# Optimization experiments

Hardware: AMD Instinct MI355X
Metric: run time of the kernel (lower is better)

The kernel has to match this reference:

```python
import jax, jax.numpy as jnp
import numpy as np

KH, KW = 3, 3
STRIDE = (1, 1)
PADDING = (1, 1)
DILATION = (1, 1)


def setup_inputs() -> dict:
    key = jax.random.key(0)
    k1, k2, k3, k4, k5 = jax.random.split(key, 5)
    B, Cin, H, W = 8, 64, 128, 128
    Cout = 64
    Ho, Wo = 128, 128  # stride 1, pad 1, k=3 -> same spatial size
    K = KH * KW
    return {
        "input": jax.random.normal(k1, (B, Cin, H, W), dtype=jnp.float32),
        "offset": jax.random.normal(k2, (B, 2 * K, Ho, Wo), dtype=jnp.float32),
        "mask": jax.random.uniform(k3, (B, K, Ho, Wo), dtype=jnp.float32),
        "weight": jax.random.normal(k4, (Cout, Cin, KH, KW), dtype=jnp.float32) * 0.05,
        "bias": jax.random.normal(k5, (Cout,), dtype=jnp.float32) * 0.05,
    }


def _deform_conv2d(x, weight, offset, mask, bias, stride, padding, dilation):
    B, Cin, H, W = x.shape
    Cout, Cing, kh, kw = weight.shape
    G = Cin // Cing                      # weight groups
    K = kh * kw
    Goff = offset.shape[1] // (2 * K)    # offset groups
    Ho, Wo = offset.shape[2], offset.shape[3]
    Cg = Cin // Goff                     # channels per offset group
    sh, sw = stride
    ph, pw = padding
    dh, dw = dilation

    # offsets laid out as (y, x) pairs per kernel tap per offset group
    off = offset.reshape(B, Goff, K, 2, Ho, Wo)
    ky = (jnp.arange(K) // kw).astype(jnp.float32) * dh   # [K]
    kx = (jnp.arange(K) % kw).astype(jnp.float32) * dw
    gy = (jnp.arange(Ho).astype(jnp.float32) * sh - ph)    # [Ho]
    gx = (jnp.arange(Wo).astype(jnp.float32) * sw - pw)
    # sampling positions: [B, Goff, K, Ho, Wo]
    py = off[:, :, :, 0] + ky[None, None, :, None, None] + gy[None, None, None, :, None]
    px = off[:, :, :, 1] + kx[None, None, :, None, None] + gx[None, None, None, None, :]

    y0 = jnp.floor(py)
    x0 = jnp.floor(px)
    ly = py - y0
    lx = px - x0
    y0i = y0.astype(jnp.int32)
    x0i = x0.astype(jnp.int32)

    x_g = x.reshape(B, Goff, Cg, H * W)

    def gather(yi, xi):
        # zero padding outside the image
        valid = (yi >= 0) & (yi < H) & (xi >= 0) & (xi < W)
        yc = jnp.clip(yi, 0, H - 1)
        xc = jnp.clip(xi, 0, W - 1)
        idx = (yc * W + xc).reshape(B, Goff, K * Ho * Wo)
        v = jnp.take_along_axis(x_g, idx[:, :, None, :], axis=3)  # [B,Goff,Cg,K*Ho*Wo]
        return v * valid.reshape(B, Goff, 1, K * Ho * Wo)

    w00 = ((1 - ly) * (1 - lx)).reshape(B, Goff, 1, K * Ho * Wo)
    w01 = ((1 - ly) * lx).reshape(B, Goff, 1, K * Ho * Wo)
    w10 = (ly * (1 - lx)).reshape(B, Goff, 1, K * Ho * Wo)
    w11 = (ly * lx).reshape(B, Goff, 1, K * Ho * Wo)

    sampled = w00 * gather(y0i, x0i)
    sampled = sampled + w01 * gather(y0i, x0i + 1)
    sampled = sampled + w10 * gather(y0i + 1, x0i)
    sampled = sampled + w11 * gather(y0i + 1, x0i + 1)
    sampled = sampled.reshape(B, Goff, Cg, K, Ho, Wo)

    if mask is not None:
        sampled = sampled * mask.reshape(B, Goff, 1, K, Ho, Wo)

    # grouped conv accumulate
    sampled = sampled.reshape(B, G, Cing, K, Ho, Wo)
    w = weight.reshape(G, Cout // G, Cing, K)
    out = jnp.einsum('gock,bgcksq->bgosq', w, sampled).reshape(B, Cout, Ho, Wo)
    if bias is not None:
        out = out + bias[None, :, None, None]
    return out


def reference(input, offset, mask, weight, bias):
    return _deform_conv2d(input, weight, offset, mask, bias, STRIDE, PADDING, DILATION)
```

## Files before the change

### kernel.cpp

```cpp
#include <hip/hip_runtime.h>
#include <hip/hip_fp16.h>

#define HH 128
#define WW 128
#define HW (HH*WW)
#define XT_BYTES ((size_t)8 * HW * 64 * 2)
#define WT_BYTES ((size_t)9 * 2 * 4 * 64 * 8 * 2)

typedef __attribute__((ext_vector_type(8))) short short8;
typedef __attribute__((ext_vector_type(4))) float f32x4;
typedef _Float16 half8 __attribute__((ext_vector_type(8)));

static __device__ __forceinline__ unsigned short f2bf(float f) {
    unsigned int u = __float_as_uint(f);
    u += 0x7fffu + ((u >> 16) & 1u);
    return (unsigned short)(u >> 16);
}
static __device__ __forceinline__ unsigned pkrtz(float lo, float hi) {
    auto r = __builtin_amdgcn_cvt_pkrtz(lo, hi);
    return *(unsigned*)&r;
}

__global__ void wtrans_kernel(const float* __restrict__ w, unsigned short* __restrict__ wt) {
    int i = blockIdx.x * 256 + threadIdx.x;
    if (i < 9 * 2 * 4 * 64 * 8) {
        int e  = i & 7;
        int l  = (i >> 3) & 63;
        int wv = (i >> 9) & 3;
        int kf = (i >> 11) & 1;
        int k  = i >> 12;
        int co = wv * 16 + (l & 15);
        int c  = kf * 32 + (l >> 4) * 8 + e;
        __half hh = __float2half_rn(w[(co * 64 + c) * 9 + k]);
        wt[i] = __half_as_ushort(hh);
    }
}

__global__ __launch_bounds__(256) void xtrans_kernel(const float* __restrict__ x,
                                                     unsigned int* __restrict__ xt32) {
    __shared__ float tile[64][65];
    const int bid = blockIdx.x;
    const int b   = bid >> 8;
    const int hw0 = (bid & 255) << 6;
    const int t   = threadIdx.x;
    #pragma unroll
    for (int i = 0; i < 16; ++i) {
        int idx = (i << 8) + t;
        int c = idx >> 6, j = idx & 63;
        tile[c][j] = x[(size_t)(((b << 6) + c) << 14) + hw0 + j];
    }
    __syncthreads();
    #pragma unroll
    for (int i = 0; i < 8; ++i) {
        int idx = (i << 8) + t;
        int cp = idx & 31, hw = idx >> 5;
        xt32[((size_t)((b << 14) + hw0 + hw) << 5) + cp] =
            pkrtz(tile[2 * cp][hw], tile[2 * cp + 1][hw]);
    }
}

__global__ __launch_bounds__(256, 6) void deform_nhwc(
    const unsigned short* __restrict__ xt,
    const float* __restrict__ off,
    const float* __restrict__ msk,
    const unsigned short* __restrict__ wt,
    const float* __restrict__ bias,
    float* __restrict__ out)
{
    __shared__ __align__(16) unsigned char smem[25600];
    ushort4* moSu = (ushort4*)(smem + 16384);
    uint2*   mwH  = (uint2*)(smem + 20992);

    const int t   = threadIdx.x;
    const int bid = blockIdx.x;
    const int b   = bid & 7;
    const int rem = bid >> 3;
    const int ho  = rem >> 1;
    const int wo0 = (rem & 1) << 6;
    const int l   = t & 63;
    const int wv  = __builtin_amdgcn_readfirstlane(t >> 6);

    for (int i = t; i < 9 * 64; i += 256) {
        int p = i & 63;
        int k = i >> 6;
        int wo = wo0 + p;
        int obase = ((b * 18 + 2 * k) * HH + ho) * WW + wo;
        float oy = off[obase];
        float ox = off[obase + HW];
        float m  = msk[((b * 9 + k) * HH + ho) * WW + wo];
        float py = oy + (float)(k / 3) + (float)(ho - 1);
        float px = ox + (float)(k % 3) + (float)(wo - 1);
        float fy = floorf(py), fx = floorf(px);
        float ly = py - fy,    lx = px - fx;
        int y0 = (int)fy, x0 = (int)fx;
        int y1 = y0 + 1,  x1 = x0 + 1;
        float vy0 = (y0 >= 0 && y0 < HH) ? 1.f : 0.f;
        float vy1 = (y1 >= 0 && y1 < HH) ? 1.f : 0.f;
        float vx0 = (x0 >= 0 && x0 < WW) ? 1.f : 0.f;
        float vx1 = (x1 >= 0 && x1 < WW) ? 1.f : 0.f;
        float w00 = (1.f - ly) * (1.f - lx) * m * vy0 * vx0;
        float w01 = (1.f - ly) * lx         * m * vy0 * vx1;
        float w10 = ly         * (1.f - lx) * m * vy1 * vx0;
        float w11 = ly         * lx         * m * vy1 * vx1;
        int yc0 = min(max(y0, 0), HH - 1), yc1 = min(max(y1, 0), HH - 1);
        int xc0 = min(max(x0, 0), WW - 1), xc1 = min(max(x1, 0), WW - 1);
        moSu[i] = make_ushort4((unsigned short)(yc0 * WW + xc0),
                               (unsigned short)(yc0 * WW + xc1),
                               (unsigned short)(yc1 * WW + xc0),
                               (unsigned short)(yc1 * WW + xc1));
        __half2 hA = __floats2half2_rn(w00, w01);
        __half2 hB = __floats2half2_rn(w10, w11);
        mwH[i] = make_uint2(*(unsigned*)&hA, *(unsigned*)&hB);
    }

    const char* ib   = (const char*)xt + (size_t)b * HW * 128;
    const int  chb   = (l & 7) << 4;
    const int  px0_  = (wv << 4) + (l >> 3);
    int st_woff[2];
    st_woff[0] = px0_ * 128 + (chb ^ ((px0_ & 7) << 4));
    st_woff[1] = st_woff[0] + 8 * 128;
    const int lq = (l >> 4) << 4;
    const int sw = (l & 7) << 4;

    uint4 g0[4], g1[4];
    half8 wtf[2][2];

    #define ISSUE_TAP(kk) {                                          \
        ushort4 ob0 = moSu[(kk) * 64 + px0_];                        \
        g0[0] = *(const uint4*)(ib + (((int)ob0.x) << 7) + chb);     \
        g0[1] = *(const uint4*)(ib + (((int)ob0.y) << 7) + chb);     \
        g0[2] = *(const uint4*)(ib + (((int)ob0.z) << 7) + chb);     \
        g0[3] = *(const uint4*)(ib + (((int)ob0.w) << 7) + chb);     \
        ushort4 ob1 = moSu[(kk) * 64 + px0_ + 8];                    \
        g1[0] = *(const uint4*)(ib + (((int)ob1.x) << 7) + chb);     \
        g1[1] = *(const uint4*)(ib + (((int)ob1.y) << 7) + chb);     \
        g1[2] = *(const uint4*)(ib + (((int)ob1.z) << 7) + chb);     \
        g1[3] = *(const uint4*)(ib + (((int)ob1.w) << 7) + chb);     \
    }

    #define CMBH(dst_, c00, c01, c10, c11) {                         \
        __half2 a_ = __hmul2(*(__half2*)&(c11), W11);                \
        a_ = __hfma2(*(__half2*)&(c10), W10, a_);                    \
        a_ = __hfma2(*(__half2*)&(c01), W01, a_);                    \
        a_ = __hfma2(*(__half2*)&(c00), W00, a_);                    \
        dst_ = *(unsigned*)&a_;                                      \
    }

    #define COMBINE_STORE(kk, dstb) {                                \
        {                                                            \
            uint2 wp = mwH[(kk) * 64 + px0_];                        \
            __half2 wab = *(__half2*)&wp.x, wcd = *(__half2*)&wp.y;  \
            __half2 W00 = __half2half2(__low2half(wab));             \
            __half2 W01 = __half2half2(__high2half(wab));            \
            __half2 W10 = __half2half2(__low2half(wcd));             \
            __half2 W11 = __half2half2(__high2half(wcd));            \
            uint4 uv;                                                \
            CMBH(uv.x, g0[0].x, g0[1].x, g0[2].x, g0[3].x)           \
            CMBH(uv.y, g0[0].y, g0[1].y, g0[2].y, g0[3].y)           \
            CMBH(uv.z, g0[0].z, g0[1].z, g0[2].z, g0[3].z)           \
            CMBH(uv.w, g0[0].w, g0[1].w, g0[2].w, g0[3].w)           \
            *(uint4*)((dstb) + st_woff[0]) = uv;                     \
        }                                                            \
        {                                                            \
            uint2 wp = mwH[(kk) * 64 + px0_ + 8];                    \
            __half2 wab = *(__half2*)&wp.x, wcd = *(__half2*)&wp.y;  \
            __half2 W00 = __half2half2(__low2half(wab));             \
            __half2 W01 = __half2half2(__high2half(wab));            \
            __half2 W10 = __half2half2(__low2half(wcd));             \
            __half2 W11 = __half2half2(__high2half(wcd));            \
            uint4 uv;                                                \
            CMBH(uv.x, g1[0].x, g1[1].x, g1[2].x, g1[3].x)           \
            CMBH(uv.y, g1[0].y, g1[1].y, g1[2].y, g1[3].y)           \
            CMBH(uv.z, g1[0].z, g1[1].z, g1[2].z, g1[3].z)           \
            CMBH(uv.w, g1[0].w, g1[1].w, g1[2].w, g1[3].w)           \
            *(uint4*)((dstb) + st_woff[1]) = uv;                     \
        }                                                            \
    }

    __syncthreads();

    ISSUE_TAP(0)
    #pragma unroll
    for (int kf = 0; kf < 2; ++kf) {
        short8 s = *(const short8*)(wt + (((kf * 4 + wv) * 64 + l) << 3));
        wtf[0][kf] = *(half8*)&s;
    }
    COMBINE_STORE(0, smem)
    __syncthreads();

    f32x4 acc[4];
    #pragma unroll
    for (int g = 0; g < 4; ++g) acc[g] = (f32x4){0.f, 0.f, 0.f, 0.f};

    #pragma unroll
    for (int s = 0; s < 9; ++s) {
        if (s < 8) {
            const int kn = s + 1;
            ISSUE_TAP(kn)
            #pragma unroll
            for (int kf = 0; kf < 2; ++kf) {
                short8 sv = *(const short8*)(wt + ((((kn * 2 + kf) * 4 + wv) * 64 + l) << 3));
                wtf[kn & 1][kf] = *(half8*)&sv;
            }
        }
        __builtin_amdgcn_sched_barrier(0);
        {
            const unsigned char* rb = smem + ((s & 1) << 13);
            #pragma unroll
            for (int g = 0; g < 4; ++g) {
                const int prow = g * 16 + (l & 15);
                short8 a0 = *(const short8*)(rb + prow * 128 + (lq ^ sw));
                short8 a1 = *(const short8*)(rb + prow * 128 + ((64 + lq) ^ sw));
                acc[g] = __builtin_amdgcn_mfma_f32_16x16x32_f16(*(half8*)&a0, wtf[s & 1][0], acc[g], 0, 0, 0);
                acc[g] = __builtin_amdgcn_mfma_f32_16x16x32_f16(*(half8*)&a1, wtf[s & 1][1], acc[g], 0, 0, 0);
            }
        }
        __builtin_amdgcn_sched_barrier(0);
        if (s < 8) {
            COMBINE_STORE(s + 1, smem + (((s + 1) & 1) << 13))
        }
        __syncthreads();
    }
    #undef ISSUE_TAP
    #undef CMBH
    #undef COMBINE_STORE

    float* out_t = (float*)smem;
    const int cb = wv << 4;
    const int co_e = cb + (l & 15);
    const float bv = bias[co_e];
    const int swE = (co_e & 15) << 4;
    #pragma unroll
    for (int g = 0; g < 4; ++g) {
        int pxb = (g << 6) + ((l >> 4) << 4);
        float4 v = make_float4(acc[g][0] + bv, acc[g][1] + bv, acc[g][2] + bv, acc[g][3] + bv);
        *(float4*)((unsigned char*)out_t + co_e * 256 + (pxb ^ swE)) = v;
    }
    __syncthreads();
    float* outb = out + (size_t)b * 64 * HW + (size_t)ho * WW + wo0;
    #pragma unroll
    for (int j = 0; j < 4; ++j) {
        int co   = (t >> 4) + (j << 4);
        int colb = (t & 15) << 4;
        float4 v = *(const float4*)((const unsigned char*)out_t + co * 256 + (colb ^ ((co & 15) << 4)));
        *(float4*)&outb[(size_t)co * HW + ((t & 15) << 2)] = v;
    }
}

__global__ __launch_bounds__(256, 4) void deform_fallback(
    const float* __restrict__ x, const float* __restrict__ off,
    const float* __restrict__ msk, const float* __restrict__ wraw,
    const float* __restrict__ bias, float* __restrict__ out)
{
    __shared__ unsigned short s_tile[2][64][68];
    __shared__ __align__(16) unsigned char meta_mem[18432];
    float4* mwS = (float4*)meta_mem;
    int4*   moS = (int4*)(meta_mem + 9216);
    float*  out_t = (float*)meta_mem;

    const int t   = threadIdx.x;
    const int bid = blockIdx.x;
    const int b   = bid & 7;
    const int rem = bid >> 3;
    const int ho  = rem >> 1;
    const int wo0 = (rem & 1) << 6;
    const int l   = t & 63;
    const int wv_id = __builtin_amdgcn_readfirstlane(t >> 6);
    const int c0  = wv_id << 4;
    const int cb  = wv_id << 4;

    short8 wtf[2][2];
    #pragma unroll
    for (int kf = 0; kf < 2; ++kf) {
        short8 f;
        int co = cb + (l & 15);
        int cbase = kf * 32 + (l >> 4) * 8;
        #pragma unroll
        for (int e = 0; e < 8; ++e) f[e] = (short)f2bf(wraw[(co * 64 + cbase + e) * 9 + 0]);
        wtf[0][kf] = f;
    }

    for (int i = t; i < 9 * 64; i += 256) {
        int p = i & 63;
        int k = i >> 6;
        int wo = wo0 + p;
        int obase = ((b * 18 + 2 * k) * HH + ho) * WW + wo;
        float oy = off[obase];
        float ox = off[obase + HW];
        float m  = msk[((b * 9 + k) * HH + ho) * WW + wo];
        float py = oy + (float)(k / 3) + (float)(ho - 1);
        float px = ox + (float)(k % 3) + (float)(wo - 1);
        float fy = floorf(py), fx = floorf(px);
        float ly = py - fy,    lx = px - fx;
        int y0 = (int)fy, x0 = (int)fx;
        int y1 = y0 + 1,  x1 = x0 + 1;
        float vy0 = (y0 >= 0 && y0 < HH) ? 1.f : 0.f;
        float vy1 = (y1 >= 0 && y1 < HH) ? 1.f : 0.f;
        float vx0 = (x0 >= 0 && x0 < WW) ? 1.f : 0.f;
        float vx1 = (x1 >= 0 && x1 < WW) ? 1.f : 0.f;
        float w00 = (1.f - ly) * (1.f - lx) * m * vy0 * vx0;
        float w01 = (1.f - ly) * lx         * m * vy0 * vx1;
        float w10 = ly         * (1.f - lx) * m * vy1 * vx0;
        float w11 = ly         * lx         * m * vy1 * vx1;
        int yc0 = min(max(y0, 0), HH - 1), yc1 = min(max(y1, 0), HH - 1);
        int xc0 = min(max(x0, 0), WW - 1), xc1 = min(max(x1, 0), WW - 1);
        mwS[i] = make_float4(w00, w01, w10, w11);
        moS[i] = make_int4(yc0 * WW + xc0, yc0 * WW + xc1,
                           yc1 * WW + xc0, yc1 * WW + xc1);
    }

    const int p = t & 63;
    const float* xb = x + (size_t)(b * 64 + c0) * HW;
    __syncthreads();

    {
        float4 wv = mwS[p];
        int4   ov = moS[p];
        const float* pc = xb;
        #pragma unroll
        for (int i = 0; i < 16; i += 4) {
            float v0 = wv.x * pc[ov.x] + wv.y * pc[ov.y] + wv.z * pc[ov.z] + wv.w * pc[ov.w]; pc += HW;
            float v1 = wv.x * pc[ov.x] + wv.y * pc[ov.y] + wv.z * pc[ov.z] + wv.w * pc[ov.w]; pc += HW;
            float v2 = wv.x * pc[ov.x] + wv.y * pc[ov.y] + wv.z * pc[ov.z] + wv.w * pc[ov.w]; pc += HW;
            float v3 = wv.x * pc[ov.x] + wv.y * pc[ov.y] + wv.z * pc[ov.z] + wv.w * pc[ov.w]; pc += HW;
            uint2 u;
            u.x = (unsigned)f2bf(v0) | ((unsigned)f2bf(v1) << 16);
            u.y = (unsigned)f2bf(v2) | ((unsigned)f2bf(v3) << 16);
            *(uint2*)&s_tile[0][p][c0 + i] = u;
        }
    }
    __syncthreads();

    f32x4 acc[4];
    #pragma unroll
    for (int g = 0; g < 4; ++g) acc[g] = (f32x4){0.f, 0.f, 0.f, 0.f};

    #pragma unroll
    for (int s = 0; s < 9; ++s) {
        if (s < 8) {
            const int kn = s + 1;
            #pragma unroll
            for (int kf = 0; kf < 2; ++kf) {
                short8 f;
                int co = cb + (l & 15);
                int cbase = kf * 32 + (l >> 4) * 8;
                #pragma unroll
                for (int e = 0; e < 8; ++e) f[e] = (short)f2bf(wraw[(co * 64 + cbase + e) * 9 + kn]);
                wtf[kn & 1][kf] = f;
            }
            float4 wv = mwS[kn * 64 + p];
            int4   ov = moS[kn * 64 + p];
            const float* pc = xb;
            #pragma unroll
            for (int i = 0; i < 16; i += 4) {
                float v0 = wv.x * pc[ov.x] + wv.y * pc[ov.y] + wv.z * pc[ov.z] + wv.w * pc[ov.w]; pc += HW;
                float v1 = wv.x * pc[ov.x] + wv.y * pc[ov.y] + wv.z * pc[ov.z] + wv.w * pc[ov.w]; pc += HW;
                float v2 = wv.x * pc[ov.x] + wv.y * pc[ov.y] + wv.z * pc[ov.z] + wv.w * pc[ov.w]; pc += HW;
                float v3 = wv.x * pc[ov.x] + wv.y * pc[ov.y] + wv.z * pc[ov.z] + wv.w * pc[ov.w]; pc += HW;
                uint2 u;
                u.x = (unsigned)f2bf(v0) | ((unsigned)f2bf(v1) << 16);
                u.y = (unsigned)f2bf(v2) | ((unsigned)f2bf(v3) << 16);
                *(uint2*)&s_tile[kn & 1][p][c0 + i] = u;
            }
        }
        #pragma unroll
        for (int g = 0; g < 4; ++g) {
            const int prow = g * 16 + (l & 15);
            const unsigned short* rp = &s_tile[s & 1][prow][(l >> 4) * 8];
            union { short8 v; unsigned long long q[2]; } ua0, ua1;
            ua0.q[0] = *(const unsigned long long*)(rp);
            ua0.q[1] = *(const unsigned long long*)(rp + 4);
            ua1.q[0] = *(const unsigned long long*)(rp + 32);
            ua1.q[1] = *(const unsigned long long*)(rp + 36);
            acc[g] = __builtin_amdgcn_mfma_f32_16x16x32_bf16(ua0.v, wtf[s & 1][0], acc[g], 0, 0, 0);
            acc[g] = __builtin_amdgcn_mfma_f32_16x16x32_bf16(ua1.v, wtf[s & 1][1], acc[g], 0, 0, 0);
        }
        __syncthreads();
    }

    const float bv = bias[cb + (l & 15)];
    #pragma unroll
    for (int g = 0; g < 4; ++g) {
        int co = cb + (l & 15);
        int pxb = g * 16 + (l >> 4) * 4;
        #pragma unroll
        for (int r = 0; r < 4; ++r)
            out_t[co * 68 + pxb + r] = acc[g][r] + bv;
    }
    __syncthreads();
    float* outb = out + (size_t)b * 64 * HW + (size_t)ho * WW + wo0;
    #pragma unroll
    for (int j = 0; j < 4; ++j) {
        int co  = (t >> 4) + j * 16;
        int px0 = (t & 15) << 2;
        float4 v = *(float4*)&out_t[co * 68 + px0];
        *(float4*)&outb[(size_t)co * HW + px0] = v;
    }
}

extern "C" void kernel_launch(void* const* d_in, const int* in_sizes, int n_in,
                              void* d_out, int out_size, void* d_ws, size_t ws_size,
                              hipStream_t stream) {
    const float* x    = (const float*)d_in[0];
    const float* off  = (const float*)d_in[1];
    const float* msk  = (const float*)d_in[2];
    const float* w    = (const float*)d_in[3];
    const float* bias = (const float*)d_in[4];
    float* out = (float*)d_out;

    const size_t need = XT_BYTES + WT_BYTES;
    if (d_ws != nullptr && ws_size >= need) {
        unsigned int*   xt32 = (unsigned int*)d_ws;
        unsigned short* wt   = (unsigned short*)((char*)d_ws + XT_BYTES);
        xtrans_kernel<<<2048, 256, 0, stream>>>(x, xt32);
        wtrans_kernel<<<144, 256, 0, stream>>>(w, wt);
        deform_nhwc<<<2048, 256, 0, stream>>>((const unsigned short*)xt32, off, msk, wt, bias, out);
    } else {
        deform_fallback<<<2048, 256, 0, stream>>>(x, off, msk, w, bias, out);
    }
}
```

Before: 48.42 us.

## Make each wave own its pixel rows and drop per-tap block barriers

Reorganizes the MFMA work split so each wave computes all 64 output channels for its own 16 pixels instead of 16 channels for all 64 pixels. Because a wave now only reads the sampled tile it wrote itself, the per-tap __syncthreads and the sched barriers are removed and each wave uses a private double-buffered LDS region. In exchange, every wave loads all eight weight fragments per tap, which raises register pressure; launch bounds are lowered from 6 to 4 blocks per CU.

```diff
diff --git a/kernel.cpp b/kernel.cpp
--- a/kernel.cpp
+++ b/kernel.cpp
@@ -59,7 +59,7 @@
     }
 }
 
-__global__ __launch_bounds__(256, 6) void deform_nhwc(
+__global__ __launch_bounds__(256, 4) void deform_nhwc(
     const unsigned short* __restrict__ xt,
     const float* __restrict__ off,
     const float* __restrict__ msk,
@@ -115,15 +115,17 @@
 
     const char* ib   = (const char*)xt + (size_t)b * HW * 128;
     const int  chb   = (l & 7) << 4;
-    const int  px0_  = (wv << 4) + (l >> 3);
+    const int  ploc  = l >> 3;
+    const int  px0_  = (wv << 4) + ploc;
+    unsigned char* wbase = smem + (wv << 12);
     int st_woff[2];
-    st_woff[0] = px0_ * 128 + (chb ^ ((px0_ & 7) << 4));
+    st_woff[0] = ploc * 128 + (chb ^ ((ploc & 7) << 4));
     st_woff[1] = st_woff[0] + 8 * 128;
     const int lq = (l >> 4) << 4;
     const int sw = (l & 7) << 4;
 
     uint4 g0[4], g1[4];
-    half8 wtf[2][2];
+    half8 wtf[8];
 
     #define ISSUE_TAP(kk) {                                          \
         ushort4 ob0 = moSu[(kk) * 64 + px0_];                        \
@@ -136,6 +138,14 @@
         g1[1] = *(const uint4*)(ib + (((int)ob1.y) << 7) + chb);     \
         g1[2] = *(const uint4*)(ib + (((int)ob1.z) << 7) + chb);     \
         g1[3] = *(const uint4*)(ib + (((int)ob1.w) << 7) + chb);     \
+    }
+
+    #define ISSUE_WTF(kk) {                                          \
+        _Pragma("unroll")                                            \
+        for (int q = 0; q < 8; ++q) {                                \
+            short8 sv = *(const short8*)(wt + ((((kk) * 8 + q) * 64 + l) << 3)); \
+            wtf[q] = *(half8*)&sv;                                   \
+        }                                                            \
     }
 
     #define CMBH(dst_, c00, c01, c10, c11) {                         \
@@ -180,13 +190,8 @@
     __syncthreads();
 
     ISSUE_TAP(0)
-    #pragma unroll
-    for (int kf = 0; kf < 2; ++kf) {
-        short8 s = *(const short8*)(wt + (((kf * 4 + wv) * 64 + l) << 3));
-        wtf[0][kf] = *(half8*)&s;
-    }
-    COMBINE_STORE(0, smem)
-    __syncthreads();
+    COMBINE_STORE(0, wbase)
+    ISSUE_WTF(0)
 
     f32x4 acc[4];
     #pragma unroll
@@ -194,46 +199,38 @@
 
     #pragma unroll
     for (int s = 0; s < 9; ++s) {
-        if (s < 8) {
-            const int kn = s + 1;
-            ISSUE_TAP(kn)
+        if (s < 8) { ISSUE_TAP(s + 1) }
+        {
+            const unsigned char* rb = wbase + ((s & 1) << 11);
+            const int arow = (l & 15) * 128;
+            short8 a0 = *(const short8*)(rb + arow + (lq ^ sw));
+            short8 a1 = *(const short8*)(rb + arow + ((64 + lq) ^ sw));
             #pragma unroll
-            for (int kf = 0; kf < 2; ++kf) {
-                short8 sv = *(const short8*)(wt + ((((kn * 2 + kf) * 4 + wv) * 64 + l) << 3));
-                wtf[kn & 1][kf] = *(half8*)&sv;
+            for (int cot = 0; cot < 4; ++cot) {
+                acc[cot] = __builtin_amdgcn_mfma_f32_16x16x32_f16(*(half8*)&a0, wtf[cot],     acc[cot], 0, 0, 0);
+                acc[cot] = __builtin_amdgcn_mfma_f32_16x16x32_f16(*(half8*)&a1, wtf[4 + cot], acc[cot], 0, 0, 0);
             }
         }
-        __builtin_amdgcn_sched_barrier(0);
-        {
-            const unsigned char* rb = smem + ((s & 1) << 13);
-            #pragma unroll
-            for (int g = 0; g < 4; ++g) {
-                const int prow = g * 16 + (l & 15);
-                short8 a0 = *(const short8*)(rb + prow * 128 + (lq ^ sw));
-                short8 a1 = *(const short8*)(rb + prow * 128 + ((64 + lq) ^ sw));
-                acc[g] = __builtin_amdgcn_mfma_f32_16x16x32_f16(*(half8*)&a0, wtf[s & 1][0], acc[g], 0, 0, 0);
-                acc[g] = __builtin_amdgcn_mfma_f32_16x16x32_f16(*(half8*)&a1, wtf[s & 1][1], acc[g], 0, 0, 0);
-            }
+        if (s < 8) {
+            ISSUE_WTF(s + 1)
+            COMBINE_STORE(s + 1, wbase + (((s + 1) & 1) << 11))
         }
-        __builtin_amdgcn_sched_barrier(0);
-        if (s < 8) {
-            COMBINE_STORE(s + 1, smem + (((s + 1) & 1) << 13))
-        }
-        __syncthreads();
     }
     #undef ISSUE_TAP
+    #undef ISSUE_WTF
     #undef CMBH
     #undef COMBINE_STORE
 
+    __syncthreads();
     float* out_t = (float*)smem;
-    const int cb = wv << 4;
-    const int co_e = cb + (l & 15);
-    const float bv = bias[co_e];
-    const int swE = (co_e & 15) << 4;
-    #pragma unroll
-    for (int g = 0; g < 4; ++g) {
-        int pxb = (g << 6) + ((l >> 4) << 4);
-        float4 v = make_float4(acc[g][0] + bv, acc[g][1] + bv, acc[g][2] + bv, acc[g][3] + bv);
+    const int pxb = (wv << 6) + ((l >> 4) << 4);
+    const int swE = (l & 15) << 4;
+    #pragma unroll
+    for (int cot = 0; cot < 4; ++cot) {
+        int co_e = (cot << 4) + (l & 15);
+        float bv = bias[co_e];
+        float4 v = make_float4(acc[cot][0] + bv, acc[cot][1] + bv,
+                               acc[cot][2] + bv, acc[cot][3] + bv);
         *(float4*)((unsigned char*)out_t + co_e * 256 + (pxb ^ swE)) = v;
     }
     __syncthreads();
```

Result: slower. 55.89 us (+15.4%).

## Deepen gather pipeline to two taps in flight with inline-asm loads and vmcnt waits

Applied to the files above, without the earlier changes.

Gathers for tap s+2 are issued while tap s+1 is combined, using two register buffers, so about two taps of global loads stay outstanding. Loads go through inline-asm global_load_dwordx4 with explicit s_waitcnt vmcnt counts and a raw s_barrier, replacing compiler-managed waits. Launch bounds drop from 6 to 3 blocks per SM to leave room for the larger register footprint. The cost is lower occupancy and fragile hand-counted vmcnt values that must match the issue order exactly.

```diff
diff --git a/kernel.cpp b/kernel.cpp
--- a/kernel.cpp
+++ b/kernel.cpp
@@ -59,7 +59,7 @@
     }
 }
 
-__global__ __launch_bounds__(256, 6) void deform_nhwc(
+__global__ __launch_bounds__(256, 3) void deform_nhwc(
     const unsigned short* __restrict__ xt,
     const float* __restrict__ off,
     const float* __restrict__ msk,
@@ -122,21 +122,34 @@
     const int lq = (l >> 4) << 4;
     const int sw = (l & 7) << 4;
 
-    uint4 g0[4], g1[4];
-    half8 wtf[2][2];
-
-    #define ISSUE_TAP(kk) {                                          \
-        ushort4 ob0 = moSu[(kk) * 64 + px0_];                        \
-        g0[0] = *(const uint4*)(ib + (((int)ob0.x) << 7) + chb);     \
-        g0[1] = *(const uint4*)(ib + (((int)ob0.y) << 7) + chb);     \
-        g0[2] = *(const uint4*)(ib + (((int)ob0.z) << 7) + chb);     \
-        g0[3] = *(const uint4*)(ib + (((int)ob0.w) << 7) + chb);     \
-        ushort4 ob1 = moSu[(kk) * 64 + px0_ + 8];                    \
-        g1[0] = *(const uint4*)(ib + (((int)ob1.x) << 7) + chb);     \
-        g1[1] = *(const uint4*)(ib + (((int)ob1.y) << 7) + chb);     \
-        g1[2] = *(const uint4*)(ib + (((int)ob1.z) << 7) + chb);     \
-        g1[3] = *(const uint4*)(ib + (((int)ob1.w) << 7) + chb);     \
-    }
+    uint4 ga[8], gb[8];
+    uint4 wtfu[2][2];
+
+    #define GLD(dst, addr) \
+        asm volatile("global_load_dwordx4 %0, %1, off" : "=v"(dst) : "v"(addr))
+
+    #define GATHER(kk, A) {                                                  \
+        ushort4 ob0 = moSu[(kk) * 64 + px0_];                                \
+        ushort4 ob1 = moSu[(kk) * 64 + px0_ + 8];                            \
+        GLD(A[0], (unsigned long long)(ib + (((int)ob0.x) << 7) + chb));     \
+        GLD(A[1], (unsigned long long)(ib + (((int)ob0.y) << 7) + chb));     \
+        GLD(A[2], (unsigned long long)(ib + (((int)ob0.z) << 7) + chb));     \
+        GLD(A[3], (unsigned long long)(ib + (((int)ob0.w) << 7) + chb));     \
+        GLD(A[4], (unsigned long long)(ib + (((int)ob1.x) << 7) + chb));     \
+        GLD(A[5], (unsigned long long)(ib + (((int)ob1.y) << 7) + chb));     \
+        GLD(A[6], (unsigned long long)(ib + (((int)ob1.z) << 7) + chb));     \
+        GLD(A[7], (unsigned long long)(ib + (((int)ob1.w) << 7) + chb));     \
+    }
+
+    #define WTFLD(kk, idx) {                                                 \
+        GLD(wtfu[idx][0], (unsigned long long)((const char*)wt + ((size_t)((((kk) * 2 + 0) * 4 + wv) * 64 + l) << 4))); \
+        GLD(wtfu[idx][1], (unsigned long long)((const char*)wt + ((size_t)((((kk) * 2 + 1) * 4 + wv) * 64 + l) << 4))); \
+    }
+
+    #define VMCNT(n)  asm volatile("s_waitcnt vmcnt(" #n ")" ::: "memory"); \
+                      __builtin_amdgcn_sched_barrier(0);
+    #define STAGE_BARRIER() asm volatile("s_waitcnt lgkmcnt(0)" ::: "memory"); \
+                            __builtin_amdgcn_s_barrier();
 
     #define CMBH(dst_, c00, c01, c10, c11) {                         \
         __half2 a_ = __hmul2(*(__half2*)&(c11), W11);                \
@@ -146,7 +159,7 @@
         dst_ = *(unsigned*)&a_;                                      \
     }
 
-    #define COMBINE_STORE(kk, dstb) {                                \
+    #define COMBINE_STORE(kk, A, dstb) {                             \
         {                                                            \
             uint2 wp = mwH[(kk) * 64 + px0_];                        \
             __half2 wab = *(__half2*)&wp.x, wcd = *(__half2*)&wp.y;  \
@@ -155,10 +168,10 @@
             __half2 W10 = __half2half2(__low2half(wcd));             \
             __half2 W11 = __half2half2(__high2half(wcd));            \
             uint4 uv;                                                \
-            CMBH(uv.x, g0[0].x, g0[1].x, g0[2].x, g0[3].x)           \
-            CMBH(uv.y, g0[0].y, g0[1].y, g0[2].y, g0[3].y)           \
-            CMBH(uv.z, g0[0].z, g0[1].z, g0[2].z, g0[3].z)           \
-            CMBH(uv.w, g0[0].w, g0[1].w, g0[2].w, g0[3].w)           \
+            CMBH(uv.x, A[0].x, A[1].x, A[2].x, A[3].x)               \
+            CMBH(uv.y, A[0].y, A[1].y, A[2].y, A[3].y)               \
+            CMBH(uv.z, A[0].z, A[1].z, A[2].z, A[3].z)               \
+            CMBH(uv.w, A[0].w, A[1].w, A[2].w, A[3].w)               \
             *(uint4*)((dstb) + st_woff[0]) = uv;                     \
         }                                                            \
         {                                                            \
@@ -169,24 +182,22 @@
             __half2 W10 = __half2half2(__low2half(wcd));             \
             __half2 W11 = __half2half2(__high2half(wcd));            \
             uint4 uv;                                                \
-            CMBH(uv.x, g1[0].x, g1[1].x, g1[2].x, g1[3].x)           \
-            CMBH(uv.y, g1[0].y, g1[1].y, g1[2].y, g1[3].y)           \
-            CMBH(uv.z, g1[0].z, g1[1].z, g1[2].z, g1[3].z)           \
-            CMBH(uv.w, g1[0].w, g1[1].w, g1[2].w, g1[3].w)           \
+            CMBH(uv.x, A[4].x, A[5].x, A[6].x, A[7].x)               \
+            CMBH(uv.y, A[4].y, A[5].y, A[6].y, A[7].y)               \
+            CMBH(uv.z, A[4].z, A[5].z, A[6].z, A[7].z)               \
+            CMBH(uv.w, A[4].w, A[5].w, A[6].w, A[7].w)               \
             *(uint4*)((dstb) + st_woff[1]) = uv;                     \
         }                                                            \
     }
 
     __syncthreads();
 
-    ISSUE_TAP(0)
-    #pragma unroll
-    for (int kf = 0; kf < 2; ++kf) {
-        short8 s = *(const short8*)(wt + (((kf * 4 + wv) * 64 + l) << 3));
-        wtf[0][kf] = *(half8*)&s;
-    }
-    COMBINE_STORE(0, smem)
-    __syncthreads();
+    GATHER(0, ga)
+    WTFLD(0, 0)
+    GATHER(1, gb)
+    VMCNT(10)
+    COMBINE_STORE(0, ga, smem)
+    STAGE_BARRIER()
 
     f32x4 acc[4];
     #pragma unroll
@@ -194,16 +205,7 @@
 
     #pragma unroll
     for (int s = 0; s < 9; ++s) {
-        if (s < 8) {
-            const int kn = s + 1;
-            ISSUE_TAP(kn)
-            #pragma unroll
-            for (int kf = 0; kf < 2; ++kf) {
-                short8 sv = *(const short8*)(wt + ((((kn * 2 + kf) * 4 + wv) * 64 + l) << 3));
-                wtf[kn & 1][kf] = *(half8*)&sv;
-            }
-        }
-        __builtin_amdgcn_sched_barrier(0);
+        if (s < 8) { VMCNT(8) } else { VMCNT(0) }
         {
             const unsigned char* rb = smem + ((s & 1) << 13);
             #pragma unroll
@@ -211,17 +213,27 @@
                 const int prow = g * 16 + (l & 15);
                 short8 a0 = *(const short8*)(rb + prow * 128 + (lq ^ sw));
                 short8 a1 = *(const short8*)(rb + prow * 128 + ((64 + lq) ^ sw));
-                acc[g] = __builtin_amdgcn_mfma_f32_16x16x32_f16(*(half8*)&a0, wtf[s & 1][0], acc[g], 0, 0, 0);
-                acc[g] = __builtin_amdgcn_mfma_f32_16x16x32_f16(*(half8*)&a1, wtf[s & 1][1], acc[g], 0, 0, 0);
+                acc[g] = __builtin_amdgcn_mfma_f32_16x16x32_f16(*(half8*)&a0, *(half8*)&wtfu[s & 1][0], acc[g], 0, 0, 0);
+                acc[g] = __builtin_amdgcn_mfma_f32_16x16x32_f16(*(half8*)&a1, *(half8*)&wtfu[s & 1][1], acc[g], 0, 0, 0);
             }
         }
-        __builtin_amdgcn_sched_barrier(0);
         if (s < 8) {
-            COMBINE_STORE(s + 1, smem + (((s + 1) & 1) << 13))
+            WTFLD(s + 1, (s + 1) & 1)
+            if ((s & 1) == 0) {
+                if (s < 7) { GATHER(s + 2, ga) VMCNT(10) } else { VMCNT(2) }
+                COMBINE_STORE(s + 1, gb, smem + (((s + 1) & 1) << 13))
+            } else {
+                if (s < 7) { GATHER(s + 2, gb) VMCNT(10) } else { VMCNT(2) }
+                COMBINE_STORE(s + 1, ga, smem + (((s + 1) & 1) << 13))
+            }
         }
-        __syncthreads();
-    }
-    #undef ISSUE_TAP
+        STAGE_BARRIER()
+    }
+    #undef GLD
+    #undef GATHER
+    #undef WTFLD
+    #undef VMCNT
+    #undef STAGE_BARRIER
     #undef CMBH
     #undef COMBINE_STORE
 
```

Result: no change. 47.98 us (-0.9%).
